# Kernel optimization log

Hardware: AMD Instinct MI355X
Metric: run time of the kernel (lower is better)

## Reference

```python
import jax, jax.numpy as jnp
import numpy as np

D_MODEL = 1024
NUM_HEADS = 16
THETA = 10000.0
B, S = 4, 2048


def setup_inputs() -> dict:
    key = jax.random.key(0)
    ks = jax.random.split(key, 5)
    scale = 1.0 / np.sqrt(D_MODEL)  # keep logits in a sane range
    return {
        "q_proj_weight": jax.random.normal(ks[0], (D_MODEL, D_MODEL), jnp.float32) * scale,
        "k_proj_weight": jax.random.normal(ks[1], (D_MODEL, D_MODEL), jnp.float32) * scale,
        "v_proj_weight": jax.random.normal(ks[2], (D_MODEL, D_MODEL), jnp.float32) * scale,
        "o_proj_weight": jax.random.normal(ks[3], (D_MODEL, D_MODEL), jnp.float32) * scale,
        "in_features": jax.random.normal(ks[4], (B, S, D_MODEL), jnp.float32),
        "token_positions": jnp.arange(S, dtype=jnp.int32),
    }


def _rope(x, cos, sin):
    # interleaved-pair RoPE: pairs are (x[..., 2i], x[..., 2i+1])
    xe = x[..., 0::2]
    xo = x[..., 1::2]
    re = xe * cos - xo * sin
    ro = xe * sin + xo * cos
    return jnp.stack([re, ro], axis=-1).reshape(x.shape)


def reference(q_proj_weight, k_proj_weight, v_proj_weight, o_proj_weight,
              in_features, token_positions):
    Bv, Sv, _ = in_features.shape
    dk = D_MODEL // NUM_HEADS
    half = dk // 2

    q = in_features @ q_proj_weight.T
    k = in_features @ k_proj_weight.T
    v = in_features @ v_proj_weight.T
    # (B, S, D) -> (B, H, S, dk)
    q = q.reshape(Bv, Sv, NUM_HEADS, dk).transpose(0, 2, 1, 3)
    k = k.reshape(Bv, Sv, NUM_HEADS, dk).transpose(0, 2, 1, 3)
    v = v.reshape(Bv, Sv, NUM_HEADS, dk).transpose(0, 2, 1, 3)

    inv_freq = 1.0 / (THETA ** (jnp.arange(half, dtype=jnp.float32) / half))
    freqs = token_positions.astype(jnp.float32)[:, None] * inv_freq[None, :]  # (S, half)
    cos, sin = jnp.cos(freqs), jnp.sin(freqs)  # broadcast over (B, H, S, half)
    q = _rope(q, cos, sin)
    k = _rope(k, cos, sin)

    scores = jnp.einsum('bhqd,bhkd->bhqk', q, k) / np.sqrt(dk).astype(np.float32)
    causal = jnp.tril(jnp.ones((Sv, Sv), dtype=bool))
    scores = jnp.where(causal, scores, -jnp.inf)
    weights = jax.nn.softmax(scores, axis=-1)
    out = jnp.einsum('bhqk,bhkd->bhqd', weights, v)
    out = out.transpose(0, 2, 1, 3).reshape(Bv, Sv, D_MODEL)
    return out @ o_proj_weight.T
```

## Files before the change

### kernel.cpp

```cpp
#include <hip/hip_runtime.h>
#include <stdint.h>
#include <math.h>

#define NH 16
#define DK 64
#define S_LEN 2048
#define BB 4
#define DM 1024
#define M_TOT (BB*S_LEN)
#define KVT 64
#define QB 128

#define BM 256
#define BN 128
#define BK 64
#define NTK (DM/BK)
#define LDS_A_BUF (BM*BK)
#define LDS_B_BUF (BN*BK)

typedef __attribute__((ext_vector_type(8))) short short8;
typedef __attribute__((ext_vector_type(4))) float floatx4;
typedef __attribute__((ext_vector_type(16))) float floatx16;

typedef const __attribute__((address_space(1))) void gas_t;
typedef __attribute__((address_space(3))) void las_t;

__device__ __forceinline__ void glds16(const void* g, void* l){
  __builtin_amdgcn_global_load_lds((gas_t*)g, (las_t*)l, 16, 0, 0);
}

#define VMCNT3() asm volatile("s_waitcnt vmcnt(3)" ::: "memory")
#define VMCNT6() asm volatile("s_waitcnt vmcnt(6)" ::: "memory")
#define VMCNT0() asm volatile("s_waitcnt vmcnt(0)" ::: "memory")
#define LGKM0()  do{ asm volatile("s_waitcnt lgkmcnt(0)" ::: "memory"); __builtin_amdgcn_sched_barrier(0); }while(0)
#define BARRIER() asm volatile("s_barrier" ::: "memory")
#define SCHEDB() __builtin_amdgcn_sched_barrier(0)

#define PLSWAP(a, b) asm volatile("v_permlane32_swap_b32 %0, %1" : "+v"(a), "+v"(b))

__device__ __forceinline__ unsigned short f2bf(float f){
  unsigned int u = __float_as_uint(f);
  u += 0x7fffu + ((u >> 16) & 1u);
  return (unsigned short)(u >> 16);
}
__device__ __forceinline__ unsigned int pk_bf_trunc(float a, float b){
  return __builtin_amdgcn_perm(__float_as_uint(b), __float_as_uint(a), 0x07060302u);
}
__device__ __forceinline__ float fast_exp2(float x){
  return __builtin_amdgcn_exp2f(x);
}

__global__ void cast_all(const float* __restrict__ X,
                         const float* __restrict__ Wq, const float* __restrict__ Wk,
                         const float* __restrict__ Wv, const float* __restrict__ Wo,
                         unsigned short* __restrict__ Xb,
                         unsigned short* __restrict__ Wqb, unsigned short* __restrict__ Wkb,
                         unsigned short* __restrict__ Wvb, unsigned short* __restrict__ Wob)
{
  int b = blockIdx.x;
  const float* s;
  unsigned short* o;
  int base;
  if (b < 8192){ s = X; o = Xb; base = b; }
  else {
    int w = (b - 8192) >> 10;
    base = (b - 8192) & 1023;
    s = (w == 0) ? Wq : (w == 1) ? Wk : (w == 2) ? Wv : Wo;
    o = (w == 0) ? Wqb : (w == 1) ? Wkb : (w == 2) ? Wvb : Wob;
  }
  int i = base * 1024 + threadIdx.x * 4;
  float4 v = *(const float4*)(s + i);
  ushort4 u;
  u.x = f2bf(v.x); u.y = f2bf(v.y); u.z = f2bf(v.z); u.w = f2bf(v.w);
  *(ushort4*)(o + i) = u;
}

__device__ __forceinline__ void stage_part(const unsigned short* __restrict__ A,
                                           const unsigned short* __restrict__ Bm,
                                           int m0, int n0, int k0,
                                           unsigned short* As, unsigned short* Bs,
                                           int tid, int part)
{
  if (part == 0){
    #pragma unroll
    for (int j = 0; j < 2; j++){
      int c = j*512 + tid;
      int r = c >> 3;
      int sl = (c & 7) ^ (r & 7);
      glds16(&A[(size_t)(m0 + r)*DM + k0 + sl*8], (char*)As + (size_t)c*16);
    }
    int c = tid;
    int r = c >> 3;
    int sl = (c & 7) ^ (r & 7);
    glds16(&Bm[(size_t)(n0 + r)*DM + k0 + sl*8], (char*)Bs + (size_t)c*16);
  } else {
    #pragma unroll
    for (int j = 2; j < 4; j++){
      int c = j*512 + tid;
      int r = c >> 3;
      int sl = (c & 7) ^ (r & 7);
      glds16(&A[(size_t)(m0 + r)*DM + k0 + sl*8], (char*)As + (size_t)c*16);
    }
    int c = 512 + tid;
    int r = c >> 3;
    int sl = (c & 7) ^ (r & 7);
    glds16(&Bm[(size_t)(n0 + r)*DM + k0 + sl*8], (char*)Bs + (size_t)c*16);
  }
}

__device__ __forceinline__ void gemm_core(const unsigned short* __restrict__ A,
                                          const unsigned short* __restrict__ Bm,
                                          int m0, int n0, unsigned short* Ls,
                                          int tid, floatx4 (&acc)[4][4])
{
  unsigned short* AsB = Ls;
  unsigned short* BsB = Ls + 3*LDS_A_BUF;
  int wave = tid >> 6, lane = tid & 63;
  int l15 = lane & 15, quad = lane >> 4;
  int wm = (wave >> 1) * 64, wn = (wave & 1) * 64;
  int s0 = quad ^ (l15 & 7);

  short8 a01[2][2], a23[2][2], b[2][4][2];

  stage_part(A, Bm, m0, n0, 0,  AsB,             BsB,             tid, 0);
  stage_part(A, Bm, m0, n0, 0,  AsB,             BsB,             tid, 1);
  stage_part(A, Bm, m0, n0, BK, AsB + LDS_A_BUF, BsB + LDS_B_BUF, tid, 0);
  stage_part(A, Bm, m0, n0, BK, AsB + LDS_A_BUF, BsB + LDS_B_BUF, tid, 1);
  VMCNT6();
  BARRIER();
  #pragma unroll
  for (int mi = 0; mi < 2; mi++){
    const unsigned short* pr = AsB + (wm + mi*16 + l15)*BK;
    a01[mi][0] = *(const short8*)(pr + s0*8);
    a01[mi][1] = *(const short8*)(pr + (s0^4)*8);
  }
  #pragma unroll
  for (int ni = 0; ni < 4; ni++){
    const unsigned short* pr = BsB + (wn + ni*16 + l15)*BK;
    b[0][ni][0] = *(const short8*)(pr + s0*8);
    b[0][ni][1] = *(const short8*)(pr + (s0^4)*8);
  }

  #pragma unroll
  for (int t = 0; t < NTK; ++t){
    const int par = t & 1, nxt = par ^ 1;
    const unsigned short* Ab  = AsB + (t % 3)*LDS_A_BUF;
    const unsigned short* Abn = AsB + ((t+1) % 3)*LDS_A_BUF;
    const unsigned short* Bbn = BsB + ((t+1) % 3)*LDS_B_BUF;
    unsigned short* Ast = AsB + ((t+2) % 3)*LDS_A_BUF;
    unsigned short* Bst = BsB + ((t+2) % 3)*LDS_B_BUF;
    const int kst = (t + 2) * BK;

    LGKM0();
    #pragma unroll
    for (int mi = 0; mi < 2; mi++){
      const unsigned short* pr = Ab + (wm + (2+mi)*16 + l15)*BK;
      a23[mi][0] = *(const short8*)(pr + s0*8);
      a23[mi][1] = *(const short8*)(pr + (s0^4)*8);
    }
    if (t + 2 < NTK) stage_part(A, Bm, m0, n0, kst, Ast, Bst, tid, 0);
    SCHEDB();
    __builtin_amdgcn_s_setprio(1);
    #pragma unroll
    for (int mi = 0; mi < 2; mi++)
      #pragma unroll
      for (int ni = 0; ni < 4; ni++){
        acc[mi][ni] = __builtin_amdgcn_mfma_f32_16x16x32_bf16(a01[mi][0], b[par][ni][0], acc[mi][ni], 0, 0, 0);
        acc[mi][ni] = __builtin_amdgcn_mfma_f32_16x16x32_bf16(a01[mi][1], b[par][ni][1], acc[mi][ni], 0, 0, 0);
      }
    __builtin_amdgcn_s_setprio(0);
    if (t + 2 < NTK)      { VMCNT3(); }
    else if (t + 1 < NTK) { VMCNT0(); }
    BARRIER();

    LGKM0();
    if (t + 1 < NTK){
      #pragma unroll
      for (int mi = 0; mi < 2; mi++){
        const unsigned short* pr = Abn + (wm + mi*16 + l15)*BK;
        a01[mi][0] = *(const short8*)(pr + s0*8);
        a01[mi][1] = *(const short8*)(pr + (s0^4)*8);
      }
      #pragma unroll
      for (int ni = 0; ni < 4; ni++){
        const unsigned short* pr = Bbn + (wn + ni*16 + l15)*BK;
        b[nxt][ni][0] = *(const short8*)(pr + s0*8);
        b[nxt][ni][1] = *(const short8*)(pr + (s0^4)*8);
      }
    }
    if (t + 2 < NTK) stage_part(A, Bm, m0, n0, kst, Ast, Bst, tid, 1);
    SCHEDB();
    __builtin_amdgcn_s_setprio(1);
    #pragma unroll
    for (int mi = 0; mi < 2; mi++)
      #pragma unroll
      for (int ni = 0; ni < 4; ni++){
        acc[2+mi][ni] = __builtin_amdgcn_mfma_f32_16x16x32_bf16(a23[mi][0], b[par][ni][0], acc[2+mi][ni], 0, 0, 0);
        acc[2+mi][ni] = __builtin_amdgcn_mfma_f32_16x16x32_bf16(a23[mi][1], b[par][ni][1], acc[2+mi][ni], 0, 0, 0);
      }
    __builtin_amdgcn_s_setprio(0);
    if (t + 1 < NTK) BARRIER();
  }
}

__global__ __launch_bounds__(512, 2) void gemm_qkv(
    const unsigned short* __restrict__ Xb,
    const unsigned short* __restrict__ Wq,
    const unsigned short* __restrict__ Wk,
    const unsigned short* __restrict__ Wv,
    const int* __restrict__ pos,
    unsigned short* __restrict__ Qo,
    unsigned short* __restrict__ Ko,
    unsigned short* __restrict__ VTo)
{
  __shared__ __align__(16) unsigned short Ls[3*LDS_A_BUF + 3*LDS_B_BUF];
  int m0 = blockIdx.x * BM;
  int n0 = blockIdx.y * BN;
  int z  = blockIdx.z;
  const unsigned short* Bmat = (z == 0) ? Wq : ((z == 1) ? Wk : Wv);
  unsigned short* Out = (z == 0) ? Qo : ((z == 1) ? Ko : VTo);

  int tid = threadIdx.x;
  floatx4 acc[4][4] = {};
  gemm_core(Xb, Bmat, m0, n0, Ls, tid, acc);

  int wave = tid >> 6, lane = tid & 63;
  int l15 = lane & 15, quad = lane >> 4;
  int wm = (wave >> 1) * 64, wn = (wave & 1) * 64;

  if (z == 2){
    #pragma unroll
    for (int mi = 0; mi < 4; mi++){
      int row0 = m0 + wm + mi * 16 + quad * 4;
      int bb2 = row0 >> 11, sQ = row0 & (S_LEN - 1);
      #pragma unroll
      for (int ni = 0; ni < 4; ni++){
        int col = n0 + wn + ni * 16 + l15;
        int h = col >> 6, d = col & 63;
        ushort4 u;
        u.x = f2bf(acc[mi][ni][0]); u.y = f2bf(acc[mi][ni][1]);
        u.z = f2bf(acc[mi][ni][2]); u.w = f2bf(acc[mi][ni][3]);
        *(ushort4*)&Out[(((size_t)bb2 * NH + h) * DK + d) * S_LEN + sQ] = u;
      }
    }
  } else {
    const float SC = (z == 0) ? 0.180336879f : 1.0f;
    #pragma unroll
    for (int mi = 0; mi < 4; mi++){
      #pragma unroll
      for (int ni = 0; ni < 4; ni++){
        int col = n0 + wn + ni * 16 + l15;
        int h = col >> 6, d = col & 63;
        int fi = d >> 1, odd = d & 1;
        float invfrev = fast_exp2(-(float)fi * (13.2877123795494f / 32.0f)) * 0.15915494309f;
        #pragma unroll
        for (int r = 0; r < 4; r++){
          int row = m0 + wm + mi * 16 + quad * 4 + r;
          int bb2 = row >> 11, s = row & (S_LEN - 1);
          float p = (float)pos[s];
          float rev = p * invfrev;
          rev = rev - floorf(rev);
          float c  = __builtin_amdgcn_cosf(rev);
          float sn = __builtin_amdgcn_sinf(rev);
          float val = acc[mi][ni][r];
          float other = __shfl_xor(val, 1);
          float outv = odd ? (other * sn + val * c) : (val * c - other * sn);
          Out[(((size_t)bb2 * NH + h) * S_LEN + s) * DK + d] = f2bf(outv * SC);
        }
      }
    }
  }
}

__global__ __launch_bounds__(512, 2) void gemm_out(
    const unsigned short* __restrict__ Ab,
    const unsigned short* __restrict__ Wo,
    float* __restrict__ Out)
{
  __shared__ __align__(16) unsigned short Ls[3*LDS_A_BUF + 3*LDS_B_BUF];
  int m0 = blockIdx.x * BM;
  int n0 = blockIdx.y * BN;

  int tid = threadIdx.x;
  floatx4 acc[4][4] = {};
  gemm_core(Ab, Wo, m0, n0, Ls, tid, acc);

  int wave = tid >> 6, lane = tid & 63;
  int l15 = lane & 15, quad = lane >> 4;
  int wm = (wave >> 1) * 64, wn = (wave & 1) * 64;

  #pragma unroll
  for (int mi = 0; mi < 4; mi++){
    #pragma unroll
    for (int ni = 0; ni < 4; ni++){
      #pragma unroll
      for (int r = 0; r < 4; r++){
        int row = m0 + wm + mi * 16 + quad * 4 + r;
        int col = n0 + wn + ni * 16 + l15;
        Out[(size_t)row * DM + col] = acc[mi][ni][r];
      }
    }
  }
}

__global__ __launch_bounds__(256, 3) void attn_kernel(
    const unsigned short* __restrict__ Qg,
    const unsigned short* __restrict__ Kg,
    const unsigned short* __restrict__ VTg,
    unsigned short* __restrict__ Ao)
{
  __shared__ __align__(16) unsigned short Ks[2][KVT * 64];
  __shared__ __align__(16) unsigned short Vs[2][DK * 64];

  int bh = blockIdx.x;
  int q0 = ((int)gridDim.y - 1 - (int)blockIdx.y) * QB;
  int tid = threadIdx.x, wave = tid >> 6, lane = tid & 63;
  int l31 = lane & 31, hi = lane >> 5;
  int qw = q0 + wave * 32;
  int qg = qw + l31;

  const unsigned short* Qb = Qg + (size_t)bh * S_LEN * DK;
  const unsigned short* Kb = Kg + (size_t)bh * S_LEN * DK;
  const unsigned short* Vb = VTg + (size_t)bh * DK * S_LEN;

  short8 qf[4];
  #pragma unroll
  for (int kc = 0; kc < 4; kc++)
    qf[kc] = *(const short8*)&Qb[(size_t)qg * DK + kc * 16 + hi * 8];

  floatx16 oA = {0.f,0.f,0.f,0.f,0.f,0.f,0.f,0.f,0.f,0.f,0.f,0.f,0.f,0.f,0.f,0.f};
  floatx16 oB = {0.f,0.f,0.f,0.f,0.f,0.f,0.f,0.f,0.f,0.f,0.f,0.f,0.f,0.f,0.f,0.f};
  float lsum = 0.f;

  int e7 = l31 & 7;
  int eoff[4];
  #pragma unroll
  for (int kc = 0; kc < 4; kc++)
    eoff[kc] = l31 * 64 + (((kc * 2 + hi) ^ e7) * 8);

  int srow = tid >> 2, sj = tid & 3;
  const unsigned short* Krow = Kb + (size_t)srow * DK + sj * 16;
  const unsigned short* Vrow = Vb + (size_t)srow * S_LEN + sj * 16;
  int ws0 = (((2 * sj)     ^ (srow & 7)) * 8) + srow * 64;
  int ws1 = (((2 * sj + 1) ^ (srow & 7)) * 8) + srow * 64;

  int nt = q0 / KVT + 2;

  short8 kr0 = *(const short8*)(Krow);
  short8 kr1 = *(const short8*)(Krow + 8);
  short8 vr0 = *(const short8*)(Vrow);
  short8 vr1 = *(const short8*)(Vrow + 8);

  for (int kt = 0; kt < nt; kt++){
    int kv0 = kt * KVT;
    int p = kt & 1;
    *(short8*)&Ks[p][ws0] = kr0;
    *(short8*)&Ks[p][ws1] = kr1;
    *(short8*)&Vs[p][ws0] = vr0;
    *(short8*)&Vs[p][ws1] = vr1;
    if (kt + 1 < nt){
      int kvn = kv0 + KVT;
      kr0 = *(const short8*)(Krow + (size_t)kvn * DK);
      kr1 = *(const short8*)(Krow + (size_t)kvn * DK + 8);
      vr0 = *(const short8*)(Vrow + kvn);
      vr1 = *(const short8*)(Vrow + kvn + 8);
    }
    LGKM0();
    BARRIER();

    #pragma unroll
    for (int sub = 0; sub < 2; sub++){
      int kvs = kv0 + sub * 32;
      if (kvs <= qw + 31){
        bool subfull = (kvs + 31 <= qw);
        floatx16 s16 = {0.f,0.f,0.f,0.f,0.f,0.f,0.f,0.f,0.f,0.f,0.f,0.f,0.f,0.f,0.f,0.f};
        #pragma unroll
        for (int kc = 0; kc < 4; kc++){
          short8 kf = *(const short8*)&Ks[p][sub * 2048 + eoff[kc]];
          s16 = __builtin_amdgcn_mfma_f32_32x32x16_bf16(kf, qf[kc], s16, 0, 0, 0);
        }
        unsigned int u[8];
        float ls = 0.f;
        #pragma unroll
        for (int j = 0; j < 8; j++){
          int row0 = ((2*j) & 3) + 8 * ((2*j) >> 2) + 4 * hi;
          float v0 = s16[2*j], v1 = s16[2*j+1];
          if (!subfull){
            v0 = (kvs + row0     > qg) ? -INFINITY : v0;
            v1 = (kvs + row0 + 1 > qg) ? -INFINITY : v1;
          }
          float p0 = fast_exp2(v0);
          float p1 = fast_exp2(v1);
          ls += p0 + p1;
          u[j] = pk_bf_trunc(p0, p1);
        }
        lsum += ls;
        PLSWAP(u[0], u[2]); PLSWAP(u[1], u[3]);
        PLSWAP(u[4], u[6]); PLSWAP(u[5], u[7]);
        union { unsigned int w[4]; short8 v; } c0, c1;
        c0.w[0] = u[0]; c0.w[1] = u[1]; c0.w[2] = u[2]; c0.w[3] = u[3];
        c1.w[0] = u[4]; c1.w[1] = u[5]; c1.w[2] = u[6]; c1.w[3] = u[7];
        short8 vf0 = *(const short8*)&Vs[p][eoff[sub*2]];
        short8 vf1 = *(const short8*)&Vs[p][eoff[sub*2+1]];
        short8 vf2 = *(const short8*)&Vs[p][2048 + eoff[sub*2]];
        short8 vf3 = *(const short8*)&Vs[p][2048 + eoff[sub*2+1]];
        oA = __builtin_amdgcn_mfma_f32_32x32x16_bf16(vf0, c0.v, oA, 0, 0, 0);
        oA = __builtin_amdgcn_mfma_f32_32x32x16_bf16(vf1, c1.v, oA, 0, 0, 0);
        oB = __builtin_amdgcn_mfma_f32_32x32x16_bf16(vf2, c0.v, oB, 0, 0, 0);
        oB = __builtin_amdgcn_mfma_f32_32x32x16_bf16(vf3, c1.v, oB, 0, 0, 0);
      }
    }
  }

  float rs = lsum + __shfl_xor(lsum, 32);
  float linv = 1.0f / rs;

  int bq = bh >> 4, hq = bh & 15;
  size_t obase = (((size_t)bq * S_LEN + qg) * NH + hq) * DK;
  #pragma unroll
  for (int g = 0; g < 4; g++){
    int d0 = 8 * g + 4 * hi;
    ushort4 ua, ub;
    ua.x = f2bf(oA[4*g+0] * linv); ua.y = f2bf(oA[4*g+1] * linv);
    ua.z = f2bf(oA[4*g+2] * linv); ua.w = f2bf(oA[4*g+3] * linv);
    ub.x = f2bf(oB[4*g+0] * linv); ub.y = f2bf(oB[4*g+1] * linv);
    ub.z = f2bf(oB[4*g+2] * linv); ub.w = f2bf(oB[4*g+3] * linv);
    *(ushort4*)&Ao[obase + d0]      = ua;
    *(ushort4*)&Ao[obase + 32 + d0] = ub;
  }
}

extern "C" void kernel_launch(void* const* d_in, const int* in_sizes, int n_in,
                              void* d_out, int out_size, void* d_ws, size_t ws_size,
                              hipStream_t stream) {
  (void)in_sizes; (void)n_in; (void)out_size; (void)ws_size;
  const float* Wq = (const float*)d_in[0];
  const float* Wk = (const float*)d_in[1];
  const float* Wv = (const float*)d_in[2];
  const float* Wo = (const float*)d_in[3];
  const float* X  = (const float*)d_in[4];
  const int* pos  = (const int*)d_in[5];
  float* out = (float*)d_out;

  char* ws = (char*)d_ws;
  const size_t MB = 1024 * 1024;
  unsigned short* Xb  = (unsigned short*)(ws);
  unsigned short* Wqb = (unsigned short*)(ws + 16 * MB);
  unsigned short* Wkb = (unsigned short*)(ws + 18 * MB);
  unsigned short* Wvb = (unsigned short*)(ws + 20 * MB);
  unsigned short* Wob = (unsigned short*)(ws + 22 * MB);
  unsigned short* Qb  = (unsigned short*)(ws + 24 * MB);
  unsigned short* Kb  = (unsigned short*)(ws + 40 * MB);
  unsigned short* Vb  = (unsigned short*)(ws + 56 * MB);
  unsigned short* Ab  = (unsigned short*)(ws + 72 * MB);

  cast_all<<<12288, 256, 0, stream>>>(X, Wq, Wk, Wv, Wo, Xb, Wqb, Wkb, Wvb, Wob);

  gemm_qkv<<<dim3(M_TOT/BM, DM/BN, 3), 512, 0, stream>>>(Xb, Wqb, Wkb, Wvb, pos, Qb, Kb, Vb);
  attn_kernel<<<dim3(64, S_LEN / QB), 256, 0, stream>>>(Qb, Kb, Vb, Ab);
  gemm_out<<<dim3(M_TOT/BM, DM/BN), 512, 0, stream>>>(Ab, Wob, out);
}
```

Baseline: 219.9 us.

## Halve GEMM K-tile to 32 and raise occupancy to four blocks per CU

Shrinks the GEMM K step from 64 to 32, which halves LDS use per block (triple-buffered A/B tiles drop from about 144KB to 72KB). The staging routine is split into separate A and B loads, and the XOR swizzle, wait counts and fragment register arrays are adjusted to match. Launch bounds are raised from 2 to 4 blocks per CU so more waves can hide latency. In exchange there are twice as many K iterations, each with barriers and waits, fewer MFMAs per barrier, and tighter register limits that could cause spills.

```diff
diff --git a/kernel.cpp b/kernel.cpp
--- a/kernel.cpp
+++ b/kernel.cpp
@@ -13,7 +13,7 @@
 
 #define BM 256
 #define BN 128
-#define BK 64
+#define BK 32
 #define NTK (DM/BK)
 #define LDS_A_BUF (BM*BK)
 #define LDS_B_BUF (BN*BK)
@@ -29,8 +29,8 @@
   __builtin_amdgcn_global_load_lds((gas_t*)g, (las_t*)l, 16, 0, 0);
 }
 
+#define VMCNT2() asm volatile("s_waitcnt vmcnt(2)" ::: "memory")
 #define VMCNT3() asm volatile("s_waitcnt vmcnt(3)" ::: "memory")
-#define VMCNT6() asm volatile("s_waitcnt vmcnt(6)" ::: "memory")
 #define VMCNT0() asm volatile("s_waitcnt vmcnt(0)" ::: "memory")
 #define LGKM0()  do{ asm volatile("s_waitcnt lgkmcnt(0)" ::: "memory"); __builtin_amdgcn_sched_barrier(0); }while(0)
 #define BARRIER() asm volatile("s_barrier" ::: "memory")
@@ -75,37 +75,24 @@
   *(ushort4*)(o + i) = u;
 }
 
-__device__ __forceinline__ void stage_part(const unsigned short* __restrict__ A,
-                                           const unsigned short* __restrict__ Bm,
-                                           int m0, int n0, int k0,
-                                           unsigned short* As, unsigned short* Bs,
-                                           int tid, int part)
-{
-  if (part == 0){
-    #pragma unroll
-    for (int j = 0; j < 2; j++){
-      int c = j*512 + tid;
-      int r = c >> 3;
-      int sl = (c & 7) ^ (r & 7);
-      glds16(&A[(size_t)(m0 + r)*DM + k0 + sl*8], (char*)As + (size_t)c*16);
-    }
-    int c = tid;
-    int r = c >> 3;
-    int sl = (c & 7) ^ (r & 7);
-    glds16(&Bm[(size_t)(n0 + r)*DM + k0 + sl*8], (char*)Bs + (size_t)c*16);
-  } else {
-    #pragma unroll
-    for (int j = 2; j < 4; j++){
-      int c = j*512 + tid;
-      int r = c >> 3;
-      int sl = (c & 7) ^ (r & 7);
-      glds16(&A[(size_t)(m0 + r)*DM + k0 + sl*8], (char*)As + (size_t)c*16);
-    }
-    int c = 512 + tid;
-    int r = c >> 3;
-    int sl = (c & 7) ^ (r & 7);
-    glds16(&Bm[(size_t)(n0 + r)*DM + k0 + sl*8], (char*)Bs + (size_t)c*16);
-  }
+__device__ __forceinline__ void stage_A(const unsigned short* __restrict__ A,
+                                        int m0, int k0, unsigned short* As, int tid)
+{
+  #pragma unroll
+  for (int j = 0; j < 2; j++){
+    int c = j*512 + tid;
+    int r = c >> 2;
+    int sl = (c & 3) ^ ((r >> 1) & 3);
+    glds16(&A[(size_t)(m0 + r)*DM + k0 + sl*8], (char*)As + (size_t)c*16);
+  }
+}
+__device__ __forceinline__ void stage_B(const unsigned short* __restrict__ Bm,
+                                        int n0, int k0, unsigned short* Bs, int tid)
+{
+  int c = tid;
+  int r = c >> 2;
+  int sl = (c & 3) ^ ((r >> 1) & 3);
+  glds16(&Bm[(size_t)(n0 + r)*DM + k0 + sl*8], (char*)Bs + (size_t)c*16);
 }
 
 __device__ __forceinline__ void gemm_core(const unsigned short* __restrict__ A,
@@ -118,30 +105,22 @@
   int wave = tid >> 6, lane = tid & 63;
   int l15 = lane & 15, quad = lane >> 4;
   int wm = (wave >> 1) * 64, wn = (wave & 1) * 64;
-  int s0 = quad ^ (l15 & 7);
-
-  short8 a01[2][2], a23[2][2], b[2][4][2];
-
-  stage_part(A, Bm, m0, n0, 0,  AsB,             BsB,             tid, 0);
-  stage_part(A, Bm, m0, n0, 0,  AsB,             BsB,             tid, 1);
-  stage_part(A, Bm, m0, n0, BK, AsB + LDS_A_BUF, BsB + LDS_B_BUF, tid, 0);
-  stage_part(A, Bm, m0, n0, BK, AsB + LDS_A_BUF, BsB + LDS_B_BUF, tid, 1);
-  VMCNT6();
+  int s0 = quad ^ ((l15 >> 1) & 3);
+
+  short8 a01[2], a23[2], b[2][4];
+
+  stage_A(A, m0, 0,  AsB, tid);             stage_B(Bm, n0, 0,  BsB, tid);
+  stage_A(A, m0, BK, AsB + LDS_A_BUF, tid); stage_B(Bm, n0, BK, BsB + LDS_B_BUF, tid);
+  VMCNT3();
   BARRIER();
   #pragma unroll
-  for (int mi = 0; mi < 2; mi++){
-    const unsigned short* pr = AsB + (wm + mi*16 + l15)*BK;
-    a01[mi][0] = *(const short8*)(pr + s0*8);
-    a01[mi][1] = *(const short8*)(pr + (s0^4)*8);
-  }
-  #pragma unroll
-  for (int ni = 0; ni < 4; ni++){
-    const unsigned short* pr = BsB + (wn + ni*16 + l15)*BK;
-    b[0][ni][0] = *(const short8*)(pr + s0*8);
-    b[0][ni][1] = *(const short8*)(pr + (s0^4)*8);
-  }
-
-  #pragma unroll
+  for (int mi = 0; mi < 2; mi++)
+    a01[mi] = *(const short8*)(AsB + (wm + mi*16 + l15)*BK + s0*8);
+  #pragma unroll
+  for (int ni = 0; ni < 4; ni++)
+    b[0][ni] = *(const short8*)(BsB + (wn + ni*16 + l15)*BK + s0*8);
+
+  #pragma unroll 2
   for (int t = 0; t < NTK; ++t){
     const int par = t & 1, nxt = par ^ 1;
     const unsigned short* Ab  = AsB + (t % 3)*LDS_A_BUF;
@@ -153,57 +132,44 @@
 
     LGKM0();
     #pragma unroll
-    for (int mi = 0; mi < 2; mi++){
-      const unsigned short* pr = Ab + (wm + (2+mi)*16 + l15)*BK;
-      a23[mi][0] = *(const short8*)(pr + s0*8);
-      a23[mi][1] = *(const short8*)(pr + (s0^4)*8);
-    }
-    if (t + 2 < NTK) stage_part(A, Bm, m0, n0, kst, Ast, Bst, tid, 0);
+    for (int mi = 0; mi < 2; mi++)
+      a23[mi] = *(const short8*)(Ab + (wm + (2+mi)*16 + l15)*BK + s0*8);
+    if (t + 2 < NTK) stage_A(A, m0, kst, Ast, tid);
     SCHEDB();
     __builtin_amdgcn_s_setprio(1);
     #pragma unroll
     for (int mi = 0; mi < 2; mi++)
       #pragma unroll
-      for (int ni = 0; ni < 4; ni++){
-        acc[mi][ni] = __builtin_amdgcn_mfma_f32_16x16x32_bf16(a01[mi][0], b[par][ni][0], acc[mi][ni], 0, 0, 0);
-        acc[mi][ni] = __builtin_amdgcn_mfma_f32_16x16x32_bf16(a01[mi][1], b[par][ni][1], acc[mi][ni], 0, 0, 0);
-      }
+      for (int ni = 0; ni < 4; ni++)
+        acc[mi][ni] = __builtin_amdgcn_mfma_f32_16x16x32_bf16(a01[mi], b[par][ni], acc[mi][ni], 0, 0, 0);
     __builtin_amdgcn_s_setprio(0);
-    if (t + 2 < NTK)      { VMCNT3(); }
+    if (t + 2 < NTK)      { VMCNT2(); }
     else if (t + 1 < NTK) { VMCNT0(); }
     BARRIER();
 
     LGKM0();
     if (t + 1 < NTK){
       #pragma unroll
-      for (int mi = 0; mi < 2; mi++){
-        const unsigned short* pr = Abn + (wm + mi*16 + l15)*BK;
-        a01[mi][0] = *(const short8*)(pr + s0*8);
-        a01[mi][1] = *(const short8*)(pr + (s0^4)*8);
-      }
-      #pragma unroll
-      for (int ni = 0; ni < 4; ni++){
-        const unsigned short* pr = Bbn + (wn + ni*16 + l15)*BK;
-        b[nxt][ni][0] = *(const short8*)(pr + s0*8);
-        b[nxt][ni][1] = *(const short8*)(pr + (s0^4)*8);
-      }
-    }
-    if (t + 2 < NTK) stage_part(A, Bm, m0, n0, kst, Ast, Bst, tid, 1);
+      for (int mi = 0; mi < 2; mi++)
+        a01[mi] = *(const short8*)(Abn + (wm + mi*16 + l15)*BK + s0*8);
+      #pragma unroll
+      for (int ni = 0; ni < 4; ni++)
+        b[nxt][ni] = *(const short8*)(Bbn + (wn + ni*16 + l15)*BK + s0*8);
+    }
+    if (t + 2 < NTK) stage_B(Bm, n0, kst, Bst, tid);
     SCHEDB();
     __builtin_amdgcn_s_setprio(1);
     #pragma unroll
     for (int mi = 0; mi < 2; mi++)
       #pragma unroll
-      for (int ni = 0; ni < 4; ni++){
-        acc[2+mi][ni] = __builtin_amdgcn_mfma_f32_16x16x32_bf16(a23[mi][0], b[par][ni][0], acc[2+mi][ni], 0, 0, 0);
-        acc[2+mi][ni] = __builtin_amdgcn_mfma_f32_16x16x32_bf16(a23[mi][1], b[par][ni][1], acc[2+mi][ni], 0, 0, 0);
-      }
+      for (int ni = 0; ni < 4; ni++)
+        acc[2+mi][ni] = __builtin_amdgcn_mfma_f32_16x16x32_bf16(a23[mi], b[par][ni], acc[2+mi][ni], 0, 0, 0);
     __builtin_amdgcn_s_setprio(0);
     if (t + 1 < NTK) BARRIER();
   }
 }
 
-__global__ __launch_bounds__(512, 2) void gemm_qkv(
+__global__ __launch_bounds__(512, 4) void gemm_qkv(
     const unsigned short* __restrict__ Xb,
     const unsigned short* __restrict__ Wq,
     const unsigned short* __restrict__ Wk,
@@ -272,7 +238,7 @@
   }
 }
 
-__global__ __launch_bounds__(512, 2) void gemm_out(
+__global__ __launch_bounds__(512, 4) void gemm_out(
     const unsigned short* __restrict__ Ab,
     const unsigned short* __restrict__ Wo,
     float* __restrict__ Out)
```

After: 252.8 us. 15.0% more time.
